# Kernel optimization log

Hardware: AMD Instinct MI355X
Metric: run time of the kernel (lower is better)

Reference implementation:

```python
import jax, jax.numpy as jnp
import numpy as np

N, R, A, F, T, O = 50000, 5, 8, 128, 2, 128
RADIUS = 1.0

def _template_vertices():
    # polar grid of template vertices in cartesian coords, shape (R, A, 2)
    radii = (np.arange(1, R + 1) / R) * RADIUS
    angles = np.linspace(0.0, 2.0 * np.pi, A, endpoint=False)
    x = radii[:, None] * np.cos(angles)[None, :]
    y = radii[:, None] * np.sin(angles)[None, :]
    return np.stack([x, y], axis=-1)

def _interp_coeffs():
    # Gaussian interpolation coefficients (concrete define_interpolation_coefficients),
    # shape (R, A, R*A), rows normalized -- constant, non-trainable (built in build()).
    v = _template_vertices().reshape(R * A, 2)
    d2 = ((v[:, None, :] - v[None, :, :]) ** 2).sum(-1)
    sigma = RADIUS / R
    w = np.exp(-d2 / (2.0 * sigma ** 2))
    w = w / w.sum(axis=1, keepdims=True)
    return w.reshape(R, A, R * A).astype(np.float32)

def setup_inputs() -> dict:
    key = jax.random.key(0)
    k1, k2, k3, k4, k5 = jax.random.split(key, 5)
    mesh_signal = jax.random.normal(k1, (N, F), dtype=jnp.float32)
    bary_w = jax.random.uniform(k2, (N, R, A, 3), dtype=jnp.float32)
    bary_w = bary_w / bary_w.sum(axis=-1, keepdims=True)  # barycentric weights sum to 1
    bary_idx = jax.random.randint(k3, (N, R, A, 3), 0, N, dtype=jnp.int32)
    glorot = lambda k, shp: jax.random.uniform(
        k, shp, jnp.float32, -1.0, 1.0) * np.sqrt(6.0 / (shp[-1] + shp[-2]))
    template_weights = glorot(k4, (A, T, O, F))  # (n_angular, templates, out, feat)
    bias = glorot(k5, (T, O))
    return {"mesh_signal": mesh_signal, "bary_w": bary_w,
            "template_weights": template_weights, "bias": bias,
            "interp_coeffs": jnp.asarray(_interp_coeffs()),
            "bary_idx": bary_idx}

def reference(mesh_signal, bary_w, template_weights, bias, interp_coeffs, bary_idx):
    # --- patch operator: barycentric gather + interpolation ---
    gathered = mesh_signal[bary_idx]                       # (N,R,A,3,F) irregular gather
    interp = (bary_w[..., None] * gathered).sum(axis=-2)   # (N,R,A,F)
    # prior: mix all R*A template-vertex signals per output template vertex
    sig = interp.reshape(-1, R * A, F)                     # (N,RA,F)
    interp = jnp.einsum('nkf,rak->nraf', sig, interp_coeffs)  # (N,R,A,F)
    # --- fold: all A rotations (rotation_delta=1), vectorized by rolling weights ---
    rots = jnp.arange(0, A, 1)                             # K = A rotations
    idx = (jnp.arange(A)[None, :] + rots[:, None]) % A     # (K,A): roll(interp,+r) == roll(W,-r)
    W_all = template_weights[idx]                          # (K,A,T,O,F)
    # TF adds bias before summing over (R,A) axes -> bias appears R*A times
    z = jnp.einsum('nraf,katof->nkto', interp, W_all) + (R * A) * bias  # (N,K,T,O)
    out = jax.nn.relu(z).sum(axis=2)                       # sum over templates -> (N,K,O)
    return out
```

## Files before the change

kernel.cpp:

```cpp
#include <hip/hip_runtime.h>
#include <hip/hip_bf16.h>
#include <stdint.h>

#define NN 50000
#define RR 5
#define AA 8
#define FF 128
#define TT 2
#define OO 128
#define KDIM 1024
#define NCOLS 2048
#define RA 40

typedef __attribute__((ext_vector_type(8))) short short8;
typedef __attribute__((ext_vector_type(4))) float f32x4;
typedef __attribute__((ext_vector_type(4))) int i32x4;

__device__ inline void gload_lds16(const void* g, void* l) {
  __builtin_amdgcn_global_load_lds(
      (const __attribute__((address_space(1))) unsigned int*)g,
      (__attribute__((address_space(3))) unsigned int*)l, 16, 0, 0);
}

__global__ void prep_kernel(const float* __restrict__ mesh,
                            const float* __restrict__ coeffs,
                            const float* __restrict__ W,
                            const float* __restrict__ bary_w,
                            const int* __restrict__ bary_idx,
                            __hip_bfloat16* __restrict__ meshq,
                            float* __restrict__ C2,
                            __hip_bfloat16* __restrict__ BmatT,
                            unsigned* __restrict__ packb,
                            int do_pack) {
  int tid = blockIdx.x * blockDim.x + threadIdx.x;
  int stride = gridDim.x * blockDim.x;
  for (int i = tid; i < NN * FF; i += stride) {
    int n = i >> 7, f = i & 127;
    int p = f >> 5, fo = f & 31;
    meshq[((long)p * NN + n) * 32 + fo] = __float2bfloat16(mesh[i]);
  }
  for (int i = tid; i < AA * RA; i += stride) {
    int a = i / RA, k = i % RA;
    float s = 0.f;
    for (int r = 0; r < RR; ++r) s += coeffs[(r * AA + a) * RA + k];
    C2[i] = s;
  }
  for (int i = tid; i < NCOLS * KDIM; i += stride) {
    int c = i >> 10, kf = i & 1023;
    int kr = c >> 8, t = (c >> 7) & 1, o = c & 127;
    int a = kf >> 7, f = kf & 127;
    int arot = (a + kr) & 7;
    BmatT[i] = __float2bfloat16(W[((arot * TT + t) * OO + o) * FF + f]);
  }
  if (do_pack) {
    for (int i = tid; i < NN * 120; i += stride) {
      __hip_bfloat16 h = __float2bfloat16(bary_w[i]);
      unsigned wb = *(unsigned short*)&h;
      packb[i] = ((unsigned)bary_idx[i] << 16) | wb;
    }
  }
}

__global__ __launch_bounds__(256) void s_pass_packed(
    const __hip_bfloat16* __restrict__ meshq,
    const unsigned* __restrict__ packb,
    const float* __restrict__ C2,
    __hip_bfloat16* __restrict__ Sout,
    int p) {
  __shared__ unsigned pk_s[16 * 120];
  __shared__ float c2_s[AA * RA];
  int tid = threadIdx.x;
  long n0 = (long)blockIdx.x * 16;
  const i32x4* psrc = (const i32x4*)(packb + n0 * 120);
  for (int i = tid; i < 480; i += 256) {
    i32x4 v = __builtin_nontemporal_load(psrc + i);
    ((i32x4*)pk_s)[i] = v;
  }
  for (int i = tid; i < AA * RA; i += 256) c2_s[i] = C2[i];
  __syncthreads();

  int g = tid >> 4;
  int fo = tid & 15;
  long n = n0 + g;
  const unsigned* pg = pk_s + g * 120;
  const char* mbase = (const char*)(meshq + (long)p * NN * 32) + fo * 4;

  float sx_acc[AA], sy_acc[AA];
#pragma unroll
  for (int a = 0; a < AA; ++a) { sx_acc[a] = 0.f; sy_acc[a] = 0.f; }

#pragma unroll 5
  for (int k = 0; k < RA; ++k) {
    float sx = 0.f, sy = 0.f;
#pragma unroll
    for (int j = 0; j < 3; ++j) {
      unsigned v = pg[k * 3 + j];
      unsigned row = v >> 16;
      float w = __uint_as_float(v << 16);
      unsigned u = *(const unsigned*)(mbase + (long)row * 64);
      sx += w * __uint_as_float(u << 16);
      sy += w * __uint_as_float(u & 0xffff0000u);
    }
#pragma unroll
    for (int a = 0; a < AA; ++a) {
      float c = c2_s[a * RA + k];
      sx_acc[a] += c * sx;
      sy_acc[a] += c * sy;
    }
  }

  long base = n * KDIM + p * 32 + fo * 2;
#pragma unroll
  for (int a = 0; a < AA; ++a) {
    __hip_bfloat16 hx = __float2bfloat16(sx_acc[a]);
    __hip_bfloat16 hy = __float2bfloat16(sy_acc[a]);
    unsigned u = (unsigned)*(unsigned short*)&hx | ((unsigned)*(unsigned short*)&hy << 16);
    __builtin_nontemporal_store(u, (unsigned*)(Sout + base + a * FF));
  }
}

__global__ __launch_bounds__(256) void s_pass_kernel(
    const __hip_bfloat16* __restrict__ meshq,
    const float* __restrict__ bary_w,
    const int* __restrict__ bary_idx,
    const float* __restrict__ C2,
    __hip_bfloat16* __restrict__ Sout,
    int p) {
  __shared__ float w_s[16 * 120];
  __shared__ int i_s[16 * 120];
  __shared__ float c2_s[AA * RA];
  int tid = threadIdx.x;
  long n0 = (long)blockIdx.x * 16;
  const f32x4* wsrc = (const f32x4*)(bary_w + n0 * 120);
  const i32x4* isrc = (const i32x4*)(bary_idx + n0 * 120);
  for (int i = tid; i < 480; i += 256) {
    f32x4 wv = __builtin_nontemporal_load(wsrc + i);
    ((f32x4*)w_s)[i] = wv;
    i32x4 iv = __builtin_nontemporal_load(isrc + i);
    ((i32x4*)i_s)[i] = iv;
  }
  for (int i = tid; i < AA * RA; i += 256) c2_s[i] = C2[i];
  __syncthreads();
  int g = tid >> 4;
  int fo = tid & 15;
  long n = n0 + g;
  const float* wg = w_s + g * 120;
  const int* ig = i_s + g * 120;
  const char* mbase = (const char*)(meshq + (long)p * NN * 32) + fo * 4;
  float sx_acc[AA], sy_acc[AA];
#pragma unroll
  for (int a = 0; a < AA; ++a) { sx_acc[a] = 0.f; sy_acc[a] = 0.f; }
#pragma unroll 5
  for (int k = 0; k < RA; ++k) {
    float sx = 0.f, sy = 0.f;
#pragma unroll
    for (int j = 0; j < 3; ++j) {
      int row = ig[k * 3 + j];
      unsigned u = *(const unsigned*)(mbase + (long)row * 64);
      float w = wg[k * 3 + j];
      sx += w * __uint_as_float(u << 16);
      sy += w * __uint_as_float(u & 0xffff0000u);
    }
#pragma unroll
    for (int a = 0; a < AA; ++a) {
      float c = c2_s[a * RA + k];
      sx_acc[a] += c * sx;
      sy_acc[a] += c * sy;
    }
  }
  long base = n * KDIM + p * 32 + fo * 2;
#pragma unroll
  for (int a = 0; a < AA; ++a) {
    __hip_bfloat16 hx = __float2bfloat16(sx_acc[a]);
    __hip_bfloat16 hy = __float2bfloat16(sy_acc[a]);
    unsigned u = (unsigned)*(unsigned short*)&hx | ((unsigned)*(unsigned short*)&hy << 16);
    __builtin_nontemporal_store(u, (unsigned*)(Sout + base + a * FF));
  }
}

__global__ __launch_bounds__(512, 1) void gemm_kernel(
    const __hip_bfloat16* __restrict__ Sm,
    const __hip_bfloat16* __restrict__ BT,
    const float* __restrict__ bias,
    float* __restrict__ out) {
  int bx = blockIdx.x;
  int by = blockIdx.y;
  int kr = by & 7;
  int mt = ((by >> 3) << 3) + bx;
  if (mt >= 196) return;
  int row0 = mt * 256;
  int col0 = kr * 256;

  int tid = threadIdx.x;
  int lane = tid & 63;
  int wid = tid >> 6;
  int wave_m = wid >> 2;
  int wave_n = wid & 3;

  __shared__ __align__(16) char lds[131072];

  long srcA[2], srcB[2];
  int dstA[2], dstB[2];
#pragma unroll
  for (int i = 0; i < 2; ++i) {
    int li = i * 512 + tid;
    int r = li >> 2, sp = li & 3;
    int sl = sp ^ ((r >> 1) & 3);
    int rowA = row0 + r;
    if (rowA >= NN) rowA = NN - 1;
    srcA[i] = (long)rowA * KDIM + sl * 8;
    dstA[i] = li * 16;
    srcB[i] = (long)(col0 + r) * KDIM + sl * 8;
    dstB[i] = 16384 + li * 16;
  }
  int offA[8], offB[4];
#pragma unroll
  for (int m = 0; m < 8; ++m) {
    int r = wave_m * 128 + m * 16 + (lane & 15);
    int phys = (lane >> 4) ^ ((r >> 1) & 3);
    offA[m] = r * 64 + phys * 16;
  }
#pragma unroll
  for (int q = 0; q < 4; ++q) {
    int c = (q >> 1) * 128 + wave_n * 32 + (q & 1) * 16 + (lane & 15);
    int phys = (lane >> 4) ^ ((c >> 1) & 3);
    offB[q] = 16384 + c * 64 + phys * 16;
  }

  f32x4 acc[8][4];
#pragma unroll
  for (int m = 0; m < 8; ++m)
#pragma unroll
    for (int q = 0; q < 4; ++q) acc[m][q] = (f32x4){0.f, 0.f, 0.f, 0.f};

#define STAGE_A(T)                                                   \
  {                                                                  \
    int b_ = ((T) & 3) * 32768;                                      \
    long k0_ = (long)(T) * 32;                                       \
    _Pragma("unroll") for (int i_ = 0; i_ < 2; ++i_)                 \
        gload_lds16(Sm + srcA[i_] + k0_, lds + b_ + dstA[i_]);       \
  }
#define STAGE_B(T)                                                   \
  {                                                                  \
    int b_ = ((T) & 3) * 32768;                                      \
    long k0_ = (long)(T) * 32;                                       \
    _Pragma("unroll") for (int i_ = 0; i_ < 2; ++i_)                 \
        gload_lds16(BT + srcB[i_] + k0_, lds + b_ + dstB[i_]);       \
  }

  STAGE_A(0) STAGE_B(0) STAGE_A(1) STAGE_B(1) STAGE_A(2) STAGE_B(2)

#define GSTEP(STP, VMSTR, DOSTAGE)                                            \
  {                                                                           \
    const char* cb = lds + ((STP) & 3) * 32768;                               \
    asm volatile("s_waitcnt " VMSTR ::: "memory");                            \
    __builtin_amdgcn_sched_barrier(0);                                        \
    __builtin_amdgcn_s_barrier();                                             \
    __builtin_amdgcn_sched_barrier(0);                                        \
    short8 aF[4], bF[4], aG[4];                                               \
    _Pragma("unroll") for (int m_ = 0; m_ < 4; ++m_)                          \
        aF[m_] = *(const short8*)(cb + offA[m_]);                             \
    _Pragma("unroll") for (int q_ = 0; q_ < 4; ++q_)                          \
        bF[q_] = *(const short8*)(cb + offB[q_]);                             \
    if (DOSTAGE) STAGE_A((STP) + 3)                                           \
    __builtin_amdgcn_s_setprio(1);                                            \
    _Pragma("unroll") for (int m_ = 0; m_ < 4; ++m_)                          \
        _Pragma("unroll") for (int q_ = 0; q_ < 4; ++q_)                      \
            acc[m_][q_] = __builtin_amdgcn_mfma_f32_16x16x32_bf16(            \
                aF[m_], bF[q_], acc[m_][q_], 0, 0, 0);                        \
    __builtin_amdgcn_s_setprio(0);                                            \
    __builtin_amdgcn_sched_barrier(0);                                        \
    __builtin_amdgcn_s_barrier();                                             \
    __builtin_amdgcn_sched_barrier(0);                                        \
    _Pragma("unroll") for (int m_ = 0; m_ < 4; ++m_)                          \
        aG[m_] = *(const short8*)(cb + offA[m_ + 4]);                         \
    if (DOSTAGE) STAGE_B((STP) + 3)                                           \
    __builtin_amdgcn_s_setprio(1);                                            \
    _Pragma("unroll") for (int m_ = 0; m_ < 4; ++m_)                          \
        _Pragma("unroll") for (int q_ = 0; q_ < 4; ++q_)                      \
            acc[m_ + 4][q_] = __builtin_amdgcn_mfma_f32_16x16x32_bf16(        \
                aG[m_], bF[q_], acc[m_ + 4][q_], 0, 0, 0);                    \
    __builtin_amdgcn_s_setprio(0);                                            \
    __builtin_amdgcn_sched_barrier(0);                                        \
  }

  for (int s = 0; s < 29; ++s) GSTEP(s, "vmcnt(8)", 1)
  GSTEP(29, "vmcnt(8)", 0)
  GSTEP(30, "vmcnt(4)", 0)
  GSTEP(31, "vmcnt(0)", 0)

  int olo = wave_n * 32 + (lane & 15);
  float b00 = 40.f * bias[olo];
  float b01 = 40.f * bias[olo + 16];
  float b10 = 40.f * bias[OO + olo];
  float b11 = 40.f * bias[OO + olo + 16];
#pragma unroll
  for (int m = 0; m < 8; ++m) {
#pragma unroll
    for (int i = 0; i < 4; ++i) {
      int node = row0 + wave_m * 128 + m * 16 + (lane >> 4) * 4 + i;
      if (node < NN) {
        float r0 = fmaxf(acc[m][0][i] + b00, 0.f) + fmaxf(acc[m][2][i] + b10, 0.f);
        float r1 = fmaxf(acc[m][1][i] + b01, 0.f) + fmaxf(acc[m][3][i] + b11, 0.f);
        long base = (long)node * 1024 + kr * 128;
        __builtin_nontemporal_store(r0, out + base + olo);
        __builtin_nontemporal_store(r1, out + base + olo + 16);
      }
    }
  }
}

extern "C" void kernel_launch(void* const* d_in, const int* in_sizes, int n_in,
                              void* d_out, int out_size, void* d_ws, size_t ws_size,
                              hipStream_t stream) {
  const float* mesh   = (const float*)d_in[0];
  const float* bary_w = (const float*)d_in[1];
  const float* W      = (const float*)d_in[2];
  const float* bias   = (const float*)d_in[3];
  const float* coeffs = (const float*)d_in[4];
  const int* bidx     = (const int*)d_in[5];
  float* out = (float*)d_out;
  char* ws = (char*)d_ws;

  __hip_bfloat16* meshq = (__hip_bfloat16*)ws;
  float* C2             = (float*)(ws + 12800000);
  __hip_bfloat16* BmatT = (__hip_bfloat16*)(ws + 12801280);
  __hip_bfloat16* Smat  = (__hip_bfloat16*)(ws + 16995584);
  unsigned* packb       = (unsigned*)(ws + 119395584);

  int do_pack = (ws_size >= 143395584UL) ? 1 : 0;

  prep_kernel<<<dim3(2048), dim3(256), 0, stream>>>(mesh, coeffs, W, bary_w, bidx,
                                                    meshq, C2, BmatT, packb, do_pack);
  if (do_pack) {
    for (int p = 0; p < 4; ++p)
      s_pass_packed<<<dim3(3125), dim3(256), 0, stream>>>(meshq, packb, C2, Smat, p);
  } else {
    for (int p = 0; p < 4; ++p)
      s_pass_kernel<<<dim3(3125), dim3(256), 0, stream>>>(meshq, bary_w, bidx, C2, Smat, p);
  }
  gemm_kernel<<<dim3(8, 200), dim3(512), 0, stream>>>(Smat, BmatT, bias, out);
}
```

Measured before the change: 435.5 us.

## Double-buffer A fragments in registers with one barrier per GEMM step

Restructures the GEMM main loop so each k-step loads the B fragments, prefetches all eight A fragments for the next LDS stage into a second register set, and issues both A and B global-to-LDS stages behind a single barrier. Before, each step had two barriers with half the MFMAs between them. The gemm launch bound now asks for two blocks per CU, and the prep kernels' inner loop unroll drops from 5 to 2. The extra fragment registers together with the tighter register cap risk heavy spilling. The 128 KB LDS per block may also stop a second block from actually fitting on a CU.

Result: no change. 430.6 us (-1.1%).

```diff
diff --git a/kernel.cpp b/kernel.cpp
--- a/kernel.cpp
+++ b/kernel.cpp
@@ -89,7 +89,7 @@
 #pragma unroll
   for (int a = 0; a < AA; ++a) { sx_acc[a] = 0.f; sy_acc[a] = 0.f; }
 
-#pragma unroll 5
+#pragma unroll 2
   for (int k = 0; k < RA; ++k) {
     float sx = 0.f, sy = 0.f;
 #pragma unroll
@@ -150,7 +150,7 @@
   float sx_acc[AA], sy_acc[AA];
 #pragma unroll
   for (int a = 0; a < AA; ++a) { sx_acc[a] = 0.f; sy_acc[a] = 0.f; }
-#pragma unroll 5
+#pragma unroll 2
   for (int k = 0; k < RA; ++k) {
     float sx = 0.f, sy = 0.f;
 #pragma unroll
@@ -178,7 +178,7 @@
   }
 }
 
-__global__ __launch_bounds__(512, 1) void gemm_kernel(
+__global__ __launch_bounds__(512, 2) void gemm_kernel(
     const __hip_bfloat16* __restrict__ Sm,
     const __hip_bfloat16* __restrict__ BT,
     const float* __restrict__ bias,
@@ -248,46 +248,53 @@
         gload_lds16(BT + srcB[i_] + k0_, lds + b_ + dstB[i_]);       \
   }
 
-  STAGE_A(0) STAGE_B(0) STAGE_A(1) STAGE_B(1) STAGE_A(2) STAGE_B(2)
-
-#define GSTEP(STP, VMSTR, DOSTAGE)                                            \
+#define GSTEP(STP, AC, AN, VMSTR, DOSTAGE, DOPREF, DOBAR)                     \
   {                                                                           \
-    const char* cb = lds + ((STP) & 3) * 32768;                               \
-    asm volatile("s_waitcnt " VMSTR ::: "memory");                            \
+    const char* cb_ = lds + ((STP) & 3) * 32768;                              \
+    const char* nb_ = lds + (((STP) + 1) & 3) * 32768;                        \
+    if (DOBAR) {                                                              \
+      asm volatile("s_waitcnt " VMSTR ::: "memory");                          \
+      __builtin_amdgcn_sched_barrier(0);                                      \
+      __builtin_amdgcn_s_barrier();                                           \
+      __builtin_amdgcn_sched_barrier(0);                                      \
+    }                                                                         \
+    short8 bC_[4];                                                            \
+    _Pragma("unroll") for (int q_ = 0; q_ < 4; ++q_)                          \
+        bC_[q_] = *(const short8*)(cb_ + offB[q_]);                           \
+    if (DOPREF) {                                                             \
+      _Pragma("unroll") for (int m_ = 0; m_ < 8; ++m_)                        \
+          AN[m_] = *(const short8*)(nb_ + offA[m_]);                          \
+    }                                                                         \
+    if (DOSTAGE) { STAGE_A((STP) + 3) STAGE_B((STP) + 3) }                    \
     __builtin_amdgcn_sched_barrier(0);                                        \
-    __builtin_amdgcn_s_barrier();                                             \
-    __builtin_amdgcn_sched_barrier(0);                                        \
-    short8 aF[4], bF[4], aG[4];                                               \
-    _Pragma("unroll") for (int m_ = 0; m_ < 4; ++m_)                          \
-        aF[m_] = *(const short8*)(cb + offA[m_]);                             \
-    _Pragma("unroll") for (int q_ = 0; q_ < 4; ++q_)                          \
-        bF[q_] = *(const short8*)(cb + offB[q_]);                             \
-    if (DOSTAGE) STAGE_A((STP) + 3)                                           \
     __builtin_amdgcn_s_setprio(1);                                            \
-    _Pragma("unroll") for (int m_ = 0; m_ < 4; ++m_)                          \
+    _Pragma("unroll") for (int m_ = 0; m_ < 8; ++m_)                          \
         _Pragma("unroll") for (int q_ = 0; q_ < 4; ++q_)                      \
             acc[m_][q_] = __builtin_amdgcn_mfma_f32_16x16x32_bf16(            \
-                aF[m_], bF[q_], acc[m_][q_], 0, 0, 0);                        \
+                AC[m_], bC_[q_], acc[m_][q_], 0, 0, 0);                       \
     __builtin_amdgcn_s_setprio(0);                                            \
     __builtin_amdgcn_sched_barrier(0);                                        \
-    __builtin_amdgcn_s_barrier();                                             \
-    __builtin_amdgcn_sched_barrier(0);                                        \
-    _Pragma("unroll") for (int m_ = 0; m_ < 4; ++m_)                          \
-        aG[m_] = *(const short8*)(cb + offA[m_ + 4]);                         \
-    if (DOSTAGE) STAGE_B((STP) + 3)                                           \
-    __builtin_amdgcn_s_setprio(1);                                            \
-    _Pragma("unroll") for (int m_ = 0; m_ < 4; ++m_)                          \
-        _Pragma("unroll") for (int q_ = 0; q_ < 4; ++q_)                      \
-            acc[m_ + 4][q_] = __builtin_amdgcn_mfma_f32_16x16x32_bf16(        \
-                aG[m_], bF[q_], acc[m_ + 4][q_], 0, 0, 0);                    \
-    __builtin_amdgcn_s_setprio(0);                                            \
-    __builtin_amdgcn_sched_barrier(0);                                        \
-  }
-
-  for (int s = 0; s < 29; ++s) GSTEP(s, "vmcnt(8)", 1)
-  GSTEP(29, "vmcnt(8)", 0)
-  GSTEP(30, "vmcnt(4)", 0)
-  GSTEP(31, "vmcnt(0)", 0)
+  }
+
+  short8 a0[8], a1[8];
+
+  STAGE_A(0) STAGE_B(0) STAGE_A(1) STAGE_B(1) STAGE_A(2) STAGE_B(2)
+  asm volatile("s_waitcnt vmcnt(8)" ::: "memory");
+  __builtin_amdgcn_sched_barrier(0);
+  __builtin_amdgcn_s_barrier();
+  __builtin_amdgcn_sched_barrier(0);
+#pragma unroll
+  for (int m = 0; m < 8; ++m) a0[m] = *(const short8*)(lds + offA[m]);
+
+  for (int s2 = 0; s2 < 14; ++s2) {
+    int s = s2 * 2;
+    GSTEP(s, a0, a1, "vmcnt(4)", 1, 1, 1)
+    GSTEP(s + 1, a1, a0, "vmcnt(4)", 1, 1, 1)
+  }
+  GSTEP(28, a0, a1, "vmcnt(4)", 1, 1, 1)
+  GSTEP(29, a1, a0, "vmcnt(4)", 0, 1, 1)
+  GSTEP(30, a0, a1, "vmcnt(0)", 0, 1, 1)
+  GSTEP(31, a1, a0, "vmcnt(0)", 0, 0, 0)
 
   int olo = wave_n * 32 + (lane & 15);
   float b00 = 40.f * bias[olo];
```

## Exploit rotation symmetry with even/odd angular split to halve GEMM work

Applied to the files above, without the earlier changes.

Splits the 8 angular positions into sum and difference halves (a and a+4), so the S matrix holds even/odd combinations and the weight matrix becomes two 512-deep halves with 4 rotations each. Each rotation pair (j, j+4) is then recovered in the epilogue as zE+zO and zE-zO. This roughly halves the GEMM FLOPs and the B-matrix size. To fit, the pipeline moves to a 3-stage LDS ring with 16 k-steps and the epilogue adds cross-lane shuffles for the template sum. It also lowers the unroll factor in the S-pass loops.

Result: slower. 964.8 us (+121.5%).

```diff
diff --git a/kernel.cpp b/kernel.cpp
--- a/kernel.cpp
+++ b/kernel.cpp
@@ -9,7 +9,7 @@
 #define TT 2
 #define OO 128
 #define KDIM 1024
-#define NCOLS 2048
+#define KB 512
 #define RA 40
 
 typedef __attribute__((ext_vector_type(8))) short short8;
@@ -28,8 +28,8 @@
                             const float* __restrict__ bary_w,
                             const int* __restrict__ bary_idx,
                             __hip_bfloat16* __restrict__ meshq,
-                            float* __restrict__ C2,
-                            __hip_bfloat16* __restrict__ BmatT,
+                            float* __restrict__ G,
+                            __hip_bfloat16* __restrict__ Bh,
                             unsigned* __restrict__ packb,
                             int do_pack) {
   int tid = blockIdx.x * blockDim.x + threadIdx.x;
@@ -40,17 +40,30 @@
     meshq[((long)p * NN + n) * 32 + fo] = __float2bfloat16(mesh[i]);
   }
   for (int i = tid; i < AA * RA; i += stride) {
-    int a = i / RA, k = i % RA;
-    float s = 0.f;
-    for (int r = 0; r < RR; ++r) s += coeffs[(r * AA + a) * RA + k];
-    C2[i] = s;
-  }
-  for (int i = tid; i < NCOLS * KDIM; i += stride) {
-    int c = i >> 10, kf = i & 1023;
-    int kr = c >> 8, t = (c >> 7) & 1, o = c & 127;
-    int a = kf >> 7, f = kf & 127;
-    int arot = (a + kr) & 7;
-    BmatT[i] = __float2bfloat16(W[((arot * TT + t) * OO + o) * FF + f]);
+    int p = i / RA, k = i % RA;
+    int a = p & 3;
+    float s1 = 0.f, s2 = 0.f;
+    for (int r = 0; r < RR; ++r) {
+      s1 += coeffs[(r * AA + a) * RA + k];
+      s2 += coeffs[(r * AA + a + 4) * RA + k];
+    }
+    G[i] = (p < 4) ? (s1 + s2) : (s1 - s2);
+  }
+  for (int i = tid; i < 2048 * KB; i += stride) {
+    int col = i >> 9, k = i & 511;
+    int half = col >> 10, c = col & 1023;
+    int o = c >> 3, t = (c >> 2) & 1, j = c & 3;
+    int a4 = k >> 7, f = k & 127;
+    int m = (a4 + j) & 3;
+    float w0 = W[((m * TT + t) * OO + o) * FF + f];
+    float w4 = W[(((m + 4) * TT + t) * OO + o) * FF + f];
+    float v;
+    if (half == 0) v = 0.5f * (w0 + w4);
+    else {
+      v = 0.5f * (w0 - w4);
+      if (a4 + j >= 4) v = -v;
+    }
+    Bh[i] = __float2bfloat16(v);
   }
   if (do_pack) {
     for (int i = tid; i < NN * 120; i += stride) {
@@ -64,11 +77,11 @@
 __global__ __launch_bounds__(256) void s_pass_packed(
     const __hip_bfloat16* __restrict__ meshq,
     const unsigned* __restrict__ packb,
-    const float* __restrict__ C2,
+    const float* __restrict__ G,
     __hip_bfloat16* __restrict__ Sout,
     int p) {
   __shared__ unsigned pk_s[16 * 120];
-  __shared__ float c2_s[AA * RA];
+  __shared__ float g_s[AA * RA];
   int tid = threadIdx.x;
   long n0 = (long)blockIdx.x * 16;
   const i32x4* psrc = (const i32x4*)(packb + n0 * 120);
@@ -76,7 +89,7 @@
     i32x4 v = __builtin_nontemporal_load(psrc + i);
     ((i32x4*)pk_s)[i] = v;
   }
-  for (int i = tid; i < AA * RA; i += 256) c2_s[i] = C2[i];
+  for (int i = tid; i < AA * RA; i += 256) g_s[i] = G[i];
   __syncthreads();
 
   int g = tid >> 4;
@@ -89,7 +102,7 @@
 #pragma unroll
   for (int a = 0; a < AA; ++a) { sx_acc[a] = 0.f; sy_acc[a] = 0.f; }
 
-#pragma unroll 5
+#pragma unroll 2
   for (int k = 0; k < RA; ++k) {
     float sx = 0.f, sy = 0.f;
 #pragma unroll
@@ -103,7 +116,7 @@
     }
 #pragma unroll
     for (int a = 0; a < AA; ++a) {
-      float c = c2_s[a * RA + k];
+      float c = g_s[a * RA + k];
       sx_acc[a] += c * sx;
       sy_acc[a] += c * sy;
     }
@@ -123,12 +136,12 @@
     const __hip_bfloat16* __restrict__ meshq,
     const float* __restrict__ bary_w,
     const int* __restrict__ bary_idx,
-    const float* __restrict__ C2,
+    const float* __restrict__ G,
     __hip_bfloat16* __restrict__ Sout,
     int p) {
   __shared__ float w_s[16 * 120];
   __shared__ int i_s[16 * 120];
-  __shared__ float c2_s[AA * RA];
+  __shared__ float g_s[AA * RA];
   int tid = threadIdx.x;
   long n0 = (long)blockIdx.x * 16;
   const f32x4* wsrc = (const f32x4*)(bary_w + n0 * 120);
@@ -139,7 +152,7 @@
     i32x4 iv = __builtin_nontemporal_load(isrc + i);
     ((i32x4*)i_s)[i] = iv;
   }
-  for (int i = tid; i < AA * RA; i += 256) c2_s[i] = C2[i];
+  for (int i = tid; i < AA * RA; i += 256) g_s[i] = G[i];
   __syncthreads();
   int g = tid >> 4;
   int fo = tid & 15;
@@ -150,7 +163,7 @@
   float sx_acc[AA], sy_acc[AA];
 #pragma unroll
   for (int a = 0; a < AA; ++a) { sx_acc[a] = 0.f; sy_acc[a] = 0.f; }
-#pragma unroll 5
+#pragma unroll 2
   for (int k = 0; k < RA; ++k) {
     float sx = 0.f, sy = 0.f;
 #pragma unroll
@@ -163,7 +176,7 @@
     }
 #pragma unroll
     for (int a = 0; a < AA; ++a) {
-      float c = c2_s[a * RA + k];
+      float c = g_s[a * RA + k];
       sx_acc[a] += c * sx;
       sy_acc[a] += c * sy;
     }
@@ -179,17 +192,17 @@
 }
 
 __global__ __launch_bounds__(512, 1) void gemm_kernel(
-    const __hip_bfloat16* __restrict__ Sm,
-    const __hip_bfloat16* __restrict__ BT,
+    const __hip_bfloat16* __restrict__ Sh,
+    const __hip_bfloat16* __restrict__ Bh,
     const float* __restrict__ bias,
     float* __restrict__ out) {
   int bx = blockIdx.x;
   int by = blockIdx.y;
-  int kr = by & 7;
+  int cb = by & 7;
   int mt = ((by >> 3) << 3) + bx;
   if (mt >= 196) return;
   int row0 = mt * 256;
-  int col0 = kr * 256;
+  int cE0 = cb * 128;
 
   int tid = threadIdx.x;
   int lane = tid & 63;
@@ -197,10 +210,10 @@
   int wave_m = wid >> 2;
   int wave_n = wid & 3;
 
-  __shared__ __align__(16) char lds[131072];
-
-  long srcA[2], srcB[2];
-  int dstA[2], dstB[2];
+  __shared__ __align__(16) char lds[147456];
+
+  long srcA[2];
+  int dstA[2];
 #pragma unroll
   for (int i = 0; i < 2; ++i) {
     int li = i * 512 + tid;
@@ -210,21 +223,28 @@
     if (rowA >= NN) rowA = NN - 1;
     srcA[i] = (long)rowA * KDIM + sl * 8;
     dstA[i] = li * 16;
-    srcB[i] = (long)(col0 + r) * KDIM + sl * 8;
-    dstB[i] = 16384 + li * 16;
-  }
-  int offA[8], offB[4];
+  }
+  long srcB;
+  int dstB;
+  {
+    int r = tid >> 2, sp = tid & 3;
+    int sl = sp ^ ((r >> 1) & 3);
+    srcB = (long)(cE0 + r) * KB + sl * 8;
+    dstB = 32768 + tid * 16;
+  }
+
+  int offAE[8], offBE[2];
 #pragma unroll
   for (int m = 0; m < 8; ++m) {
     int r = wave_m * 128 + m * 16 + (lane & 15);
     int phys = (lane >> 4) ^ ((r >> 1) & 3);
-    offA[m] = r * 64 + phys * 16;
-  }
-#pragma unroll
-  for (int q = 0; q < 4; ++q) {
-    int c = (q >> 1) * 128 + wave_n * 32 + (q & 1) * 16 + (lane & 15);
+    offAE[m] = r * 64 + phys * 16;
+  }
+#pragma unroll
+  for (int q = 0; q < 2; ++q) {
+    int c = wave_n * 32 + q * 16 + (lane & 15);
     int phys = (lane >> 4) ^ ((c >> 1) & 3);
-    offB[q] = 16384 + c * 64 + phys * 16;
+    offBE[q] = 32768 + c * 64 + phys * 16;
   }
 
   f32x4 acc[8][4];
@@ -233,78 +253,98 @@
 #pragma unroll
     for (int q = 0; q < 4; ++q) acc[m][q] = (f32x4){0.f, 0.f, 0.f, 0.f};
 
-#define STAGE_A(T)                                                   \
-  {                                                                  \
-    int b_ = ((T) & 3) * 32768;                                      \
-    long k0_ = (long)(T) * 32;                                       \
-    _Pragma("unroll") for (int i_ = 0; i_ < 2; ++i_)                 \
-        gload_lds16(Sm + srcA[i_] + k0_, lds + b_ + dstA[i_]);       \
-  }
-#define STAGE_B(T)                                                   \
-  {                                                                  \
-    int b_ = ((T) & 3) * 32768;                                      \
-    long k0_ = (long)(T) * 32;                                       \
-    _Pragma("unroll") for (int i_ = 0; i_ < 2; ++i_)                 \
-        gload_lds16(BT + srcB[i_] + k0_, lds + b_ + dstB[i_]);       \
-  }
-
-  STAGE_A(0) STAGE_B(0) STAGE_A(1) STAGE_B(1) STAGE_A(2) STAGE_B(2)
+#define STAGE(T)                                                              \
+  {                                                                           \
+    char* base_ = lds + ((T) % 3) * 49152;                                    \
+    long k0_ = (long)(T) * 32;                                                \
+    _Pragma("unroll") for (int i_ = 0; i_ < 2; ++i_)                          \
+        gload_lds16(Sh + srcA[i_] + k0_, base_ + dstA[i_]);                   \
+    _Pragma("unroll") for (int i_ = 0; i_ < 2; ++i_)                          \
+        gload_lds16(Sh + srcA[i_] + 512 + k0_, base_ + 16384 + dstA[i_]);     \
+    gload_lds16(Bh + srcB + k0_, base_ + dstB);                               \
+    gload_lds16(Bh + srcB + (long)1024 * KB + k0_, base_ + 8192 + dstB);      \
+  }
 
 #define GSTEP(STP, VMSTR, DOSTAGE)                                            \
   {                                                                           \
-    const char* cb = lds + ((STP) & 3) * 32768;                               \
+    const char* cbuf = lds + ((STP) % 3) * 49152;                             \
     asm volatile("s_waitcnt " VMSTR ::: "memory");                            \
     __builtin_amdgcn_sched_barrier(0);                                        \
     __builtin_amdgcn_s_barrier();                                             \
     __builtin_amdgcn_sched_barrier(0);                                        \
-    short8 aF[4], bF[4], aG[4];                                               \
-    _Pragma("unroll") for (int m_ = 0; m_ < 4; ++m_)                          \
-        aF[m_] = *(const short8*)(cb + offA[m_]);                             \
-    _Pragma("unroll") for (int q_ = 0; q_ < 4; ++q_)                          \
-        bF[q_] = *(const short8*)(cb + offB[q_]);                             \
-    if (DOSTAGE) STAGE_A((STP) + 3)                                           \
+    short8 bE[2], bO[2], aE[8], aO[8];                                        \
+    _Pragma("unroll") for (int q_ = 0; q_ < 2; ++q_) {                        \
+      bE[q_] = *(const short8*)(cbuf + offBE[q_]);                            \
+      bO[q_] = *(const short8*)(cbuf + offBE[q_] + 8192);                     \
+    }                                                                         \
+    _Pragma("unroll") for (int m_ = 0; m_ < 8; ++m_) {                        \
+      aE[m_] = *(const short8*)(cbuf + offAE[m_]);                            \
+      aO[m_] = *(const short8*)(cbuf + offAE[m_] + 16384);                    \
+    }                                                                         \
+    if (DOSTAGE) STAGE((STP) + 2)                                             \
     __builtin_amdgcn_s_setprio(1);                                            \
-    _Pragma("unroll") for (int m_ = 0; m_ < 4; ++m_)                          \
-        _Pragma("unroll") for (int q_ = 0; q_ < 4; ++q_)                      \
-            acc[m_][q_] = __builtin_amdgcn_mfma_f32_16x16x32_bf16(            \
-                aF[m_], bF[q_], acc[m_][q_], 0, 0, 0);                        \
+    _Pragma("unroll") for (int m_ = 0; m_ < 8; ++m_) {                        \
+      acc[m_][0] = __builtin_amdgcn_mfma_f32_16x16x32_bf16(aE[m_], bE[0],     \
+                                                           acc[m_][0], 0, 0, 0); \
+      acc[m_][1] = __builtin_amdgcn_mfma_f32_16x16x32_bf16(aE[m_], bE[1],     \
+                                                           acc[m_][1], 0, 0, 0); \
+      acc[m_][2] = __builtin_amdgcn_mfma_f32_16x16x32_bf16(aO[m_], bO[0],     \
+                                                           acc[m_][2], 0, 0, 0); \
+      acc[m_][3] = __builtin_amdgcn_mfma_f32_16x16x32_bf16(aO[m_], bO[1],     \
+                                                           acc[m_][3], 0, 0, 0); \
+    }                                                                         \
     __builtin_amdgcn_s_setprio(0);                                            \
     __builtin_amdgcn_sched_barrier(0);                                        \
-    __builtin_amdgcn_s_barrier();                                             \
-    __builtin_amdgcn_sched_barrier(0);                                        \
-    _Pragma("unroll") for (int m_ = 0; m_ < 4; ++m_)                          \
-        aG[m_] = *(const short8*)(cb + offA[m_ + 4]);                         \
-    if (DOSTAGE) STAGE_B((STP) + 3)                                           \
-    __builtin_amdgcn_s_setprio(1);                                            \
-    _Pragma("unroll") for (int m_ = 0; m_ < 4; ++m_)                          \
-        _Pragma("unroll") for (int q_ = 0; q_ < 4; ++q_)                      \
-            acc[m_ + 4][q_] = __builtin_amdgcn_mfma_f32_16x16x32_bf16(        \
-                aG[m_], bF[q_], acc[m_ + 4][q_], 0, 0, 0);                    \
-    __builtin_amdgcn_s_setprio(0);                                            \
-    __builtin_amdgcn_sched_barrier(0);                                        \
-  }
-
-  for (int s = 0; s < 29; ++s) GSTEP(s, "vmcnt(8)", 1)
-  GSTEP(29, "vmcnt(8)", 0)
-  GSTEP(30, "vmcnt(4)", 0)
-  GSTEP(31, "vmcnt(0)", 0)
-
-  int olo = wave_n * 32 + (lane & 15);
-  float b00 = 40.f * bias[olo];
-  float b01 = 40.f * bias[olo + 16];
-  float b10 = 40.f * bias[OO + olo];
-  float b11 = 40.f * bias[OO + olo + 16];
+  }
+
+  STAGE(0) STAGE(1)
+  GSTEP(0, "vmcnt(6)", 1)
+  GSTEP(1, "vmcnt(6)", 1)
+  GSTEP(2, "vmcnt(6)", 1)
+  GSTEP(3, "vmcnt(6)", 1)
+  GSTEP(4, "vmcnt(6)", 1)
+  GSTEP(5, "vmcnt(6)", 1)
+  GSTEP(6, "vmcnt(6)", 1)
+  GSTEP(7, "vmcnt(6)", 1)
+  GSTEP(8, "vmcnt(6)", 1)
+  GSTEP(9, "vmcnt(6)", 1)
+  GSTEP(10, "vmcnt(6)", 1)
+  GSTEP(11, "vmcnt(6)", 1)
+  GSTEP(12, "vmcnt(6)", 1)
+  GSTEP(13, "vmcnt(6)", 1)
+  GSTEP(14, "vmcnt(6)", 0)
+  GSTEP(15, "vmcnt(0)", 0)
+
+  int c = lane & 15;
+  int t = (c >> 2) & 1;
+  int j = c & 3;
+  float bq[2];
+#pragma unroll
+  for (int q = 0; q < 2; ++q) {
+    int o = cb * 16 + wave_n * 4 + q * 2 + (c >> 3);
+    bq[q] = 40.f * bias[t * OO + o];
+  }
 #pragma unroll
   for (int m = 0; m < 8; ++m) {
 #pragma unroll
-    for (int i = 0; i < 4; ++i) {
-      int node = row0 + wave_m * 128 + m * 16 + (lane >> 4) * 4 + i;
-      if (node < NN) {
-        float r0 = fmaxf(acc[m][0][i] + b00, 0.f) + fmaxf(acc[m][2][i] + b10, 0.f);
-        float r1 = fmaxf(acc[m][1][i] + b01, 0.f) + fmaxf(acc[m][3][i] + b11, 0.f);
-        long base = (long)node * 1024 + kr * 128;
-        __builtin_nontemporal_store(r0, out + base + olo);
-        __builtin_nontemporal_store(r1, out + base + olo + 16);
+    for (int q = 0; q < 2; ++q) {
+      int o = cb * 16 + wave_n * 4 + q * 2 + (c >> 3);
+#pragma unroll
+      for (int i = 0; i < 4; ++i) {
+        float zE = acc[m][q][i];
+        float zO = acc[m][q + 2][i];
+        float rlo = fmaxf(zE + zO + bq[q], 0.f);
+        float rhi = fmaxf(zE - zO + bq[q], 0.f);
+        rlo += __shfl_xor(rlo, 4);
+        rhi += __shfl_xor(rhi, 4);
+        if (!(lane & 4)) {
+          int node = row0 + wave_m * 128 + m * 16 + (lane >> 4) * 4 + i;
+          if (node < NN) {
+            long base = (long)node * 1024;
+            __builtin_nontemporal_store(rlo, out + base + j * 128 + o);
+            __builtin_nontemporal_store(rhi, out + base + (j + 4) * 128 + o);
+          }
+        }
       }
     }
   }
@@ -323,21 +363,21 @@
   char* ws = (char*)d_ws;
 
   __hip_bfloat16* meshq = (__hip_bfloat16*)ws;
-  float* C2             = (float*)(ws + 12800000);
-  __hip_bfloat16* BmatT = (__hip_bfloat16*)(ws + 12801280);
+  float* G              = (float*)(ws + 12800000);
+  __hip_bfloat16* Bh    = (__hip_bfloat16*)(ws + 12801280);
   __hip_bfloat16* Smat  = (__hip_bfloat16*)(ws + 16995584);
   unsigned* packb       = (unsigned*)(ws + 119395584);
 
   int do_pack = (ws_size >= 143395584UL) ? 1 : 0;
 
   prep_kernel<<<dim3(2048), dim3(256), 0, stream>>>(mesh, coeffs, W, bary_w, bidx,
-                                                    meshq, C2, BmatT, packb, do_pack);
+                                                    meshq, G, Bh, packb, do_pack);
   if (do_pack) {
     for (int p = 0; p < 4; ++p)
-      s_pass_packed<<<dim3(3125), dim3(256), 0, stream>>>(meshq, packb, C2, Smat, p);
+      s_pass_packed<<<dim3(3125), dim3(256), 0, stream>>>(meshq, packb, G, Smat, p);
   } else {
     for (int p = 0; p < 4; ++p)
-      s_pass_kernel<<<dim3(3125), dim3(256), 0, stream>>>(meshq, bary_w, bidx, C2, Smat, p);
-  }
-  gemm_kernel<<<dim3(8, 200), dim3(512), 0, stream>>>(Smat, BmatT, bias, out);
-}
+      s_pass_kernel<<<dim3(3125), dim3(256), 0, stream>>>(meshq, bary_w, bidx, G, Smat, p);
+  }
+  gemm_kernel<<<dim3(8, 200), dim3(512), 0, stream>>>(Smat, Bh, bias, out);
+}
```
